# Kernel optimization log

Measured on AMD Instinct MI355X. Metric: run time of the kernel, lower is better.

The kernel has to match this reference:

```python
import jax, jax.numpy as jnp
import numpy as np

EPS = 1e-5  # nn.LayerNorm default

def _conv1x1(x, W):
    # x: (B,C,H,W), W: (O,C) -> (B,O,H,W)
    return jnp.einsum('bchw,oc->bohw', x, W)

def setup_inputs() -> dict:
    key = jax.random.key(0)
    kx, k1, k2, k3, k4, k5 = jax.random.split(key, 6)
    B, C, H, W = 16, 512, 64, 64
    inner = C // 2
    s = 1.0 / np.sqrt(C)
    return {
        'x':   jax.random.normal(kx, (B, C, H, W), dtype=jnp.float32),
        'Wsq': jax.random.normal(k1, (inner, C), dtype=jnp.float32) * s,
        'Wsv': jax.random.normal(k2, (inner, C), dtype=jnp.float32) * s,
        'Wcq': jax.random.normal(k3, (1, C), dtype=jnp.float32) * s,
        'Wcv': jax.random.normal(k4, (inner, C), dtype=jnp.float32) * s,
        'Wcz': jax.random.normal(k5, (C, inner), dtype=jnp.float32) * (1.0 / np.sqrt(inner)),
        'gamma': jnp.ones((C,), dtype=jnp.float32),
        'beta':  jnp.zeros((C,), dtype=jnp.float32),
    }

def _channel_pool(x, Wcq, Wcv, Wcz, gamma, beta):
    B, C, H, W = x.shape
    HW = H * W
    # channel_q: 1x1 conv to 1 channel -> (B, HW), softmax over HW
    cm = jnp.einsum('bchw,c->bhw', x, Wcq[0]).reshape(B, HW)
    cm = jax.nn.softmax(cm, axis=-1)                      # (B, HW)
    # channel_v: (B, inner, HW)
    iv = _conv1x1(x, Wcv).reshape(B, Wcv.shape[0], HW)
    context = jnp.einsum('bkn,bn->bk', iv, cm)            # (B, inner)
    z = jnp.einsum('bk,ok->bo', context, Wcz)             # (B, out)
    mu = jnp.mean(z, axis=-1, keepdims=True)
    var = jnp.mean((z - mu) ** 2, axis=-1, keepdims=True)
    zn = (z - mu) * jax.lax.rsqrt(var + EPS) * gamma + beta
    mask = jax.nn.sigmoid(zn)[:, :, None, None]           # (B, out, 1, 1)
    return x * mask

def _spatial_pool(x, Wsq, Wsv):
    B, C, H, W = x.shape
    HW = H * W
    g = _conv1x1(x, Wsq)                                  # (B, inner, H, W)
    avg = jnp.mean(g, axis=(2, 3))                        # (B, inner)
    avg = jax.nn.softmax(avg, axis=-1)                    # softmax over inner channels
    theta = _conv1x1(x, Wsv).reshape(B, Wsv.shape[0], HW) # (B, inner, HW)
    ctx = jnp.einsum('bk,bkn->bn', avg, theta).reshape(B, 1, H, W)
    return x * jax.nn.sigmoid(ctx)

def reference(x, Wsq, Wsv, Wcq, Wcv, Wcz, gamma, beta):
    # layout='parallel'
    ch = _channel_pool(x, Wcq, Wcv, Wcz, gamma, beta)
    sp = _spatial_pool(x, Wsq, Wsv)
    return ch + sp
```

## Files before the change

kernel.cpp:

```cpp
#include <hip/hip_runtime.h>
#include <math.h>

#define BB 16
#define CC 512
#define HWN 4096
#define INNER 256
#define EPSV 1e-5f

__device__ __forceinline__ float wave_sum(float s) {
    for (int off = 32; off; off >>= 1) s += __shfl_down(s, off);
    return s;
}
__device__ __forceinline__ float block_sum(float v, volatile float* s_red) {
    for (int off = 32; off; off >>= 1) v += __shfl_down(v, off);
    __syncthreads();
    if ((threadIdx.x & 63) == 0) s_red[threadIdx.x >> 6] = v;
    __syncthreads();
    return s_red[0] + s_red[1] + s_red[2] + s_red[3];
}
__device__ __forceinline__ float block_max(float v, volatile float* s_red) {
    for (int off = 32; off; off >>= 1) v = fmaxf(v, __shfl_down(v, off));
    __syncthreads();
    if ((threadIdx.x & 63) == 0) s_red[threadIdx.x >> 6] = v;
    __syncthreads();
    return fmaxf(fmaxf(s_red[0], s_red[1]), fmaxf(s_red[2], s_red[3]));
}
__device__ __forceinline__ float fsigmoid(float v) {
    return __builtin_amdgcn_rcpf(1.f + __expf(-v));
}

__global__ __launch_bounds__(256) void k1_pass(
    const float* __restrict__ x, const float* __restrict__ wcq,
    float* __restrict__ cm_logits, float* __restrict__ xsum)
{
    const int t = threadIdx.x, lane = t & 63, w = t >> 6;
    const int hw0 = blockIdx.x * 1024;
    const int c0  = blockIdx.y * 64;
    const int b   = blockIdx.z;
    __shared__ float s_w[64];
    __shared__ float s_red[4][1024];
    if (t < 64) s_w[t] = wcq[c0 + t];
    __syncthreads();

    const float* xb = x + ((size_t)b * CC + c0) * HWN + hw0 + lane * 4;
    float4 cm0 = {0,0,0,0}, cm1 = cm0, cm2 = cm0, cm3 = cm0;
    #pragma unroll 4
    for (int ci = 0; ci < 16; ++ci) {
        const int cl = w + ci * 4;
        const float* p = xb + (size_t)cl * HWN;
        float4 v0 = *(const float4*)(p);
        float4 v1 = *(const float4*)(p + 256);
        float4 v2 = *(const float4*)(p + 512);
        float4 v3 = *(const float4*)(p + 768);
        const float wc = s_w[cl];
        cm0.x = fmaf(v0.x, wc, cm0.x); cm0.y = fmaf(v0.y, wc, cm0.y);
        cm0.z = fmaf(v0.z, wc, cm0.z); cm0.w = fmaf(v0.w, wc, cm0.w);
        cm1.x = fmaf(v1.x, wc, cm1.x); cm1.y = fmaf(v1.y, wc, cm1.y);
        cm1.z = fmaf(v1.z, wc, cm1.z); cm1.w = fmaf(v1.w, wc, cm1.w);
        cm2.x = fmaf(v2.x, wc, cm2.x); cm2.y = fmaf(v2.y, wc, cm2.y);
        cm2.z = fmaf(v2.z, wc, cm2.z); cm2.w = fmaf(v2.w, wc, cm2.w);
        cm3.x = fmaf(v3.x, wc, cm3.x); cm3.y = fmaf(v3.y, wc, cm3.y);
        cm3.z = fmaf(v3.z, wc, cm3.z); cm3.w = fmaf(v3.w, wc, cm3.w);
        float s = (((v0.x+v0.y)+(v0.z+v0.w)) + ((v1.x+v1.y)+(v1.z+v1.w)))
                + (((v2.x+v2.y)+(v2.z+v2.w)) + ((v3.x+v3.y)+(v3.z+v3.w)));
        s = wave_sum(s);
        if (lane == 0) atomicAdd(&xsum[b * CC + c0 + cl], s);
    }
    *(float4*)&s_red[w][      lane*4] = cm0;
    *(float4*)&s_red[w][256 + lane*4] = cm1;
    *(float4*)&s_red[w][512 + lane*4] = cm2;
    *(float4*)&s_red[w][768 + lane*4] = cm3;
    __syncthreads();
    float4 r0 = *(float4*)&s_red[0][t*4];
    float4 r1 = *(float4*)&s_red[1][t*4];
    float4 r2 = *(float4*)&s_red[2][t*4];
    float4 r3 = *(float4*)&s_red[3][t*4];
    float* cp = cm_logits + b * HWN + hw0 + t * 4;
    atomicAdd(cp + 0, (r0.x + r1.x) + (r2.x + r3.x));
    atomicAdd(cp + 1, (r0.y + r1.y) + (r2.y + r3.y));
    atomicAdd(cp + 2, (r0.z + r1.z) + (r2.z + r3.z));
    atomicAdd(cp + 3, (r0.w + r1.w) + (r2.w + r3.w));
}

__global__ __launch_bounds__(256) void k2a_cmstats(
    const float* __restrict__ cm_logits, float* __restrict__ cmstats)
{
    const int b = blockIdx.x, t = threadIdx.x;
    __shared__ float s_red[4];
    const float* cl = cm_logits + b * HWN;
    float lmax = -1e30f;
    #pragma unroll 4
    for (int i = t; i < HWN; i += 256) lmax = fmaxf(lmax, cl[i]);
    lmax = block_max(lmax, s_red);
    float lsum = 0.f;
    #pragma unroll 4
    for (int i = t; i < HWN; i += 256) lsum += __expf(cl[i] - lmax);
    lsum = block_sum(lsum, s_red);
    if (t == 0) {
        cmstats[2 * b]     = lmax;
        cmstats[2 * b + 1] = __builtin_amdgcn_rcpf(lsum);
    }
}

__global__ __launch_bounds__(256) void k_mv512(
    const float* __restrict__ W, const float* __restrict__ v,
    float* __restrict__ y, float scale)
{
    const int b = blockIdx.x, t = threadIdx.x, lane = t & 63, w = t >> 6;
    const int k0 = blockIdx.y * 64;
    __shared__ float s_v[CC];
    s_v[t]       = v[b * CC + t];
    s_v[t + 256] = v[b * CC + t + 256];
    __syncthreads();
    float4 x0 = *(const float4*)&s_v[lane * 4];
    float4 x1 = *(const float4*)&s_v[256 + lane * 4];
    #pragma unroll 8
    for (int i = 0; i < 16; ++i) {
        const int k = k0 + w * 16 + i;
        const float* row = W + (size_t)k * CC + lane * 4;
        float4 q0 = *(const float4*)(row);
        float4 q1 = *(const float4*)(row + 256);
        float s = fmaf(q0.x,x0.x, fmaf(q0.y,x0.y, fmaf(q0.z,x0.z, q0.w*x0.w)))
                + fmaf(q1.x,x1.x, fmaf(q1.y,x1.y, fmaf(q1.z,x1.z, q1.w*x1.w)));
        s = wave_sum(s);
        if (lane == 0) y[b * INNER + k] = s * scale;
    }
}

__global__ __launch_bounds__(256) void k2c_wsv(
    const float* __restrict__ Wsv, const float* __restrict__ avg_logits,
    float* __restrict__ wsv_eff)
{
    const int b = blockIdx.x, t = threadIdx.x;
    const int c = blockIdx.y * 256 + t;
    __shared__ float s_red[4];
    __shared__ float s_avg[INNER];
    float a = avg_logits[b * INNER + t];
    float m = block_max(a, s_red);
    float e = __expf(a - m);
    float s2 = block_sum(e, s_red);
    s_avg[t] = e * __builtin_amdgcn_rcpf(s2);
    __syncthreads();
    float acc = 0.f;
    #pragma unroll 8
    for (int k = 0; k < INNER; ++k)
        acc = fmaf(s_avg[k], Wsv[(size_t)k * CC + c], acc);
    wsv_eff[b * CC + c] = acc;
}

__global__ __launch_bounds__(256) void k3_pass(
    const float* __restrict__ x, const float* __restrict__ wsv_eff,
    const float* __restrict__ cm_logits, const float* __restrict__ cmstats,
    float* __restrict__ ctx, float* __restrict__ xw)
{
    const int t = threadIdx.x, lane = t & 63, w = t >> 6;
    const int hw0 = blockIdx.x * 1024;
    const int c0  = blockIdx.y * 64;
    const int b   = blockIdx.z;
    __shared__ float s_w[64];
    __shared__ float s_red[4][1024];
    if (t < 64) s_w[t] = wsv_eff[b * CC + c0 + t];
    __syncthreads();

    const float cmax = cmstats[2 * b], crinv = cmstats[2 * b + 1];
    const float* mb = cm_logits + b * HWN + hw0 + lane * 4;
    float4 m0 = *(const float4*)(mb);
    float4 m1 = *(const float4*)(mb + 256);
    float4 m2 = *(const float4*)(mb + 512);
    float4 m3 = *(const float4*)(mb + 768);
    m0.x = __expf(m0.x - cmax) * crinv; m0.y = __expf(m0.y - cmax) * crinv;
    m0.z = __expf(m0.z - cmax) * crinv; m0.w = __expf(m0.w - cmax) * crinv;
    m1.x = __expf(m1.x - cmax) * crinv; m1.y = __expf(m1.y - cmax) * crinv;
    m1.z = __expf(m1.z - cmax) * crinv; m1.w = __expf(m1.w - cmax) * crinv;
    m2.x = __expf(m2.x - cmax) * crinv; m2.y = __expf(m2.y - cmax) * crinv;
    m2.z = __expf(m2.z - cmax) * crinv; m2.w = __expf(m2.w - cmax) * crinv;
    m3.x = __expf(m3.x - cmax) * crinv; m3.y = __expf(m3.y - cmax) * crinv;
    m3.z = __expf(m3.z - cmax) * crinv; m3.w = __expf(m3.w - cmax) * crinv;

    const float* xb = x + ((size_t)b * CC + c0) * HWN + hw0 + lane * 4;
    float4 a0 = {0,0,0,0}, a1 = a0, a2 = a0, a3 = a0;
    #pragma unroll 4
    for (int ci = 0; ci < 16; ++ci) {
        const int cl = w + ci * 4;
        const float* p = xb + (size_t)cl * HWN;
        float4 v0 = *(const float4*)(p);
        float4 v1 = *(const float4*)(p + 256);
        float4 v2 = *(const float4*)(p + 512);
        float4 v3 = *(const float4*)(p + 768);
        const float wc = s_w[cl];
        a0.x = fmaf(v0.x, wc, a0.x); a0.y = fmaf(v0.y, wc, a0.y);
        a0.z = fmaf(v0.z, wc, a0.z); a0.w = fmaf(v0.w, wc, a0.w);
        a1.x = fmaf(v1.x, wc, a1.x); a1.y = fmaf(v1.y, wc, a1.y);
        a1.z = fmaf(v1.z, wc, a1.z); a1.w = fmaf(v1.w, wc, a1.w);
        a2.x = fmaf(v2.x, wc, a2.x); a2.y = fmaf(v2.y, wc, a2.y);
        a2.z = fmaf(v2.z, wc, a2.z); a2.w = fmaf(v2.w, wc, a2.w);
        a3.x = fmaf(v3.x, wc, a3.x); a3.y = fmaf(v3.y, wc, a3.y);
        a3.z = fmaf(v3.z, wc, a3.z); a3.w = fmaf(v3.w, wc, a3.w);
        float s = fmaf(v0.x,m0.x, fmaf(v0.y,m0.y, fmaf(v0.z,m0.z, v0.w*m0.w)))
                + fmaf(v1.x,m1.x, fmaf(v1.y,m1.y, fmaf(v1.z,m1.z, v1.w*m1.w)))
                + fmaf(v2.x,m2.x, fmaf(v2.y,m2.y, fmaf(v2.z,m2.z, v2.w*m2.w)))
                + fmaf(v3.x,m3.x, fmaf(v3.y,m3.y, fmaf(v3.z,m3.z, v3.w*m3.w)));
        s = wave_sum(s);
        if (lane == 0) atomicAdd(&xw[b * CC + c0 + cl], s);
    }
    *(float4*)&s_red[w][      lane*4] = a0;
    *(float4*)&s_red[w][256 + lane*4] = a1;
    *(float4*)&s_red[w][512 + lane*4] = a2;
    *(float4*)&s_red[w][768 + lane*4] = a3;
    __syncthreads();
    float4 r0 = *(float4*)&s_red[0][t*4];
    float4 r1 = *(float4*)&s_red[1][t*4];
    float4 r2 = *(float4*)&s_red[2][t*4];
    float4 r3 = *(float4*)&s_red[3][t*4];
    float* cp = ctx + b * HWN + hw0 + t * 4;
    atomicAdd(cp + 0, (r0.x + r1.x) + (r2.x + r3.x));
    atomicAdd(cp + 1, (r0.y + r1.y) + (r2.y + r3.y));
    atomicAdd(cp + 2, (r0.z + r1.z) + (r2.z + r3.z));
    atomicAdd(cp + 3, (r0.w + r1.w) + (r2.w + r3.w));
}

__global__ __launch_bounds__(256) void k4b_z(
    const float* __restrict__ Wcz, const float* __restrict__ context,
    float* __restrict__ zbuf)
{
    const int b = blockIdx.x, t = threadIdx.x, lane = t & 63, w = t >> 6;
    const int o0 = blockIdx.y * 128;
    __shared__ float s_c[INNER];
    s_c[t] = context[b * INNER + t];
    __syncthreads();
    float4 cv = *(const float4*)&s_c[lane * 4];
    #pragma unroll 8
    for (int i = 0; i < 32; ++i) {
        const int o = o0 + w * 32 + i;
        float4 q = *(const float4*)(Wcz + (size_t)o * INNER + lane * 4);
        float s = fmaf(q.x,cv.x, fmaf(q.y,cv.y, fmaf(q.z,cv.z, q.w*cv.w)));
        s = wave_sum(s);
        if (lane == 0) zbuf[b * CC + o] = s;
    }
}

__global__ __launch_bounds__(256) void k4c_ln(
    const float* __restrict__ gamma, const float* __restrict__ beta,
    const float* __restrict__ zbuf, const float* __restrict__ ctx,
    float* __restrict__ mask, float* __restrict__ ctx_sig)
{
    const int b = blockIdx.x, t = threadIdx.x;
    __shared__ float s_red[4];
    float z0 = zbuf[b * CC + t], z1 = zbuf[b * CC + t + 256];
    float mu = block_sum(z0 + z1, s_red) * (1.f / CC);
    float d0 = z0 - mu, d1 = z1 - mu;
    float var = block_sum(d0 * d0 + d1 * d1, s_red) * (1.f / CC);
    float rstd = rsqrtf(var + EPSV);
    float zn0 = fmaf(d0 * rstd, gamma[t], beta[t]);
    float zn1 = fmaf(d1 * rstd, gamma[t + 256], beta[t + 256]);
    mask[b * CC + t]       = fsigmoid(zn0);
    mask[b * CC + t + 256] = fsigmoid(zn1);
    const float* ci = ctx + b * HWN;
    float* cs = ctx_sig + b * HWN;
    #pragma unroll 4
    for (int i = t; i < HWN; i += 256) cs[i] = fsigmoid(ci[i]);
}

__global__ __launch_bounds__(256) void k5_final(
    const float* __restrict__ x, const float* __restrict__ ctx_sig,
    const float* __restrict__ mask, float* __restrict__ out)
{
    const int t  = threadIdx.x;
    const int hw = blockIdx.x * 1024 + 4 * t;
    const int c  = blockIdx.y;
    const int b  = blockIdx.z;
    const float m = mask[b * CC + c];
    float4 s = *(const float4*)(ctx_sig + b * HWN + hw);
    const size_t base = ((size_t)b * CC + c) * HWN + hw;
    float4 xv = *(const float4*)(x + base);
    float4 o;
    o.x = xv.x * (m + s.x);
    o.y = xv.y * (m + s.y);
    o.z = xv.z * (m + s.z);
    o.w = xv.w * (m + s.w);
    *(float4*)(out + base) = o;
}

extern "C" void kernel_launch(void* const* d_in, const int* in_sizes, int n_in,
                              void* d_out, int out_size, void* d_ws, size_t ws_size,
                              hipStream_t stream) {
    const float* x     = (const float*)d_in[0];
    const float* Wsq   = (const float*)d_in[1];
    const float* Wsv   = (const float*)d_in[2];
    const float* Wcq   = (const float*)d_in[3];
    const float* Wcv   = (const float*)d_in[4];
    const float* Wcz   = (const float*)d_in[5];
    const float* gamma = (const float*)d_in[6];
    const float* beta  = (const float*)d_in[7];
    float* out = (float*)d_out;
    float* ws  = (float*)d_ws;

    float* cm_logits  = ws;
    float* ctx        = ws + 65536;
    float* xsum       = ws + 131072;
    float* xw         = ws + 139264;
    float* avg_logits = ws + 147456;
    float* wsv_eff    = ws + 151552;
    float* maskbuf    = ws + 159744;
    float* zbuf       = ws + 167936;
    float* context    = ws + 176128;
    float* ctx_sig    = ws + 180224;
    float* cmstats    = ws + 245760;

    hipMemsetAsync(d_ws, 0, 147456 * sizeof(float), stream);

    k1_pass<<<dim3(4, 8, BB), 256, 0, stream>>>(x, Wcq, cm_logits, xsum);
    k2a_cmstats<<<BB, 256, 0, stream>>>(cm_logits, cmstats);
    k_mv512<<<dim3(BB, 4), 256, 0, stream>>>(Wsq, xsum, avg_logits, 1.0f / HWN);
    k2c_wsv<<<dim3(BB, 2), 256, 0, stream>>>(Wsv, avg_logits, wsv_eff);
    k3_pass<<<dim3(4, 8, BB), 256, 0, stream>>>(x, wsv_eff, cm_logits, cmstats, ctx, xw);
    k_mv512<<<dim3(BB, 4), 256, 0, stream>>>(Wcv, xw, context, 1.0f);
    k4b_z<<<dim3(BB, 4), 256, 0, stream>>>(Wcz, context, zbuf);
    k4c_ln<<<BB, 256, 0, stream>>>(gamma, beta, zbuf, ctx, maskbuf, ctx_sig);
    k5_final<<<dim3(4, CC, BB), 256, 0, stream>>>(x, ctx_sig, maskbuf, out);
}
```

Measured before the change: 361.0 us.

## Replace atomics with partial buffers and fuse small stages into fewer kernels

The streaming passes over x now write per-block partial sums to disjoint buffers instead of using atomicAdd, which also removes the workspace memset. Blocks are retiled to 256 channels by 256 pixels. The softmax stats, the Wsq matvec, the channel softmax and the Wsv projection are fused into one per-batch kernel, and likewise the Wcv and Wcz matvecs and the LayerNorm. The final kernel now computes the spatial sigmoid inline and handles 16 channels per block. Launches and atomic contention go down, but the fused per-batch kernels run on only 16 blocks, so they have little parallelism.

```diff
diff --git a/kernel.cpp b/kernel.cpp
--- a/kernel.cpp
+++ b/kernel.cpp
@@ -29,256 +29,220 @@
     return __builtin_amdgcn_rcpf(1.f + __expf(-v));
 }
 
-__global__ __launch_bounds__(256) void k1_pass(
+__global__ __launch_bounds__(256) void kA(
     const float* __restrict__ x, const float* __restrict__ wcq,
-    float* __restrict__ cm_logits, float* __restrict__ xsum)
+    float* __restrict__ cm_part, float* __restrict__ xsum_part)
 {
     const int t = threadIdx.x, lane = t & 63, w = t >> 6;
-    const int hw0 = blockIdx.x * 1024;
-    const int c0  = blockIdx.y * 64;
+    const int hw0 = blockIdx.x * 256;
+    const int ch  = blockIdx.y;
+    const int c0  = ch * 256;
     const int b   = blockIdx.z;
-    __shared__ float s_w[64];
-    __shared__ float s_red[4][1024];
-    if (t < 64) s_w[t] = wcq[c0 + t];
-    __syncthreads();
-
+    __shared__ float s_w[256];
+    __shared__ float s_cm[4][256];
+    s_w[t] = wcq[c0 + t];
+    __syncthreads();
     const float* xb = x + ((size_t)b * CC + c0) * HWN + hw0 + lane * 4;
-    float4 cm0 = {0,0,0,0}, cm1 = cm0, cm2 = cm0, cm3 = cm0;
-    #pragma unroll 4
-    for (int ci = 0; ci < 16; ++ci) {
+    float* xsp = xsum_part + ((size_t)b * 16 + blockIdx.x) * CC + c0;
+    float4 acc = {0.f, 0.f, 0.f, 0.f};
+    #pragma unroll 8
+    for (int ci = 0; ci < 64; ++ci) {
         const int cl = w + ci * 4;
-        const float* p = xb + (size_t)cl * HWN;
-        float4 v0 = *(const float4*)(p);
-        float4 v1 = *(const float4*)(p + 256);
-        float4 v2 = *(const float4*)(p + 512);
-        float4 v3 = *(const float4*)(p + 768);
+        float4 v = *(const float4*)(xb + (size_t)cl * HWN);
         const float wc = s_w[cl];
-        cm0.x = fmaf(v0.x, wc, cm0.x); cm0.y = fmaf(v0.y, wc, cm0.y);
-        cm0.z = fmaf(v0.z, wc, cm0.z); cm0.w = fmaf(v0.w, wc, cm0.w);
-        cm1.x = fmaf(v1.x, wc, cm1.x); cm1.y = fmaf(v1.y, wc, cm1.y);
-        cm1.z = fmaf(v1.z, wc, cm1.z); cm1.w = fmaf(v1.w, wc, cm1.w);
-        cm2.x = fmaf(v2.x, wc, cm2.x); cm2.y = fmaf(v2.y, wc, cm2.y);
-        cm2.z = fmaf(v2.z, wc, cm2.z); cm2.w = fmaf(v2.w, wc, cm2.w);
-        cm3.x = fmaf(v3.x, wc, cm3.x); cm3.y = fmaf(v3.y, wc, cm3.y);
-        cm3.z = fmaf(v3.z, wc, cm3.z); cm3.w = fmaf(v3.w, wc, cm3.w);
-        float s = (((v0.x+v0.y)+(v0.z+v0.w)) + ((v1.x+v1.y)+(v1.z+v1.w)))
-                + (((v2.x+v2.y)+(v2.z+v2.w)) + ((v3.x+v3.y)+(v3.z+v3.w)));
-        s = wave_sum(s);
-        if (lane == 0) atomicAdd(&xsum[b * CC + c0 + cl], s);
-    }
-    *(float4*)&s_red[w][      lane*4] = cm0;
-    *(float4*)&s_red[w][256 + lane*4] = cm1;
-    *(float4*)&s_red[w][512 + lane*4] = cm2;
-    *(float4*)&s_red[w][768 + lane*4] = cm3;
-    __syncthreads();
-    float4 r0 = *(float4*)&s_red[0][t*4];
-    float4 r1 = *(float4*)&s_red[1][t*4];
-    float4 r2 = *(float4*)&s_red[2][t*4];
-    float4 r3 = *(float4*)&s_red[3][t*4];
-    float* cp = cm_logits + b * HWN + hw0 + t * 4;
-    atomicAdd(cp + 0, (r0.x + r1.x) + (r2.x + r3.x));
-    atomicAdd(cp + 1, (r0.y + r1.y) + (r2.y + r3.y));
-    atomicAdd(cp + 2, (r0.z + r1.z) + (r2.z + r3.z));
-    atomicAdd(cp + 3, (r0.w + r1.w) + (r2.w + r3.w));
-}
-
-__global__ __launch_bounds__(256) void k2a_cmstats(
-    const float* __restrict__ cm_logits, float* __restrict__ cmstats)
-{
-    const int b = blockIdx.x, t = threadIdx.x;
+        acc.x = fmaf(v.x, wc, acc.x); acc.y = fmaf(v.y, wc, acc.y);
+        acc.z = fmaf(v.z, wc, acc.z); acc.w = fmaf(v.w, wc, acc.w);
+        float s = (v.x + v.y) + (v.z + v.w);
+        s = wave_sum(s);
+        if (lane == 0) xsp[cl] = s;
+    }
+    *(float4*)&s_cm[w][lane * 4] = acc;
+    __syncthreads();
+    cm_part[((size_t)b * 2 + ch) * HWN + hw0 + t] =
+        (s_cm[0][t] + s_cm[1][t]) + (s_cm[2][t] + s_cm[3][t]);
+}
+
+__global__ __launch_bounds__(256) void kB(
+    const float* __restrict__ Wsq, const float* __restrict__ Wsv,
+    const float* __restrict__ cm_part, const float* __restrict__ xsum_part,
+    float* __restrict__ cmstats, float* __restrict__ wsv_eff)
+{
+    const int b = blockIdx.x, t = threadIdx.x, lane = t & 63, w = t >> 6;
     __shared__ float s_red[4];
-    const float* cl = cm_logits + b * HWN;
+    __shared__ float s_x[CC];
+    __shared__ float s_avg[INNER];
+    __shared__ float s_sm[INNER];
+    float a0 = 0.f, a1 = 0.f;
+    const float* xp = xsum_part + (size_t)b * 16 * CC;
+    #pragma unroll
+    for (int blk = 0; blk < 16; ++blk) {
+        a0 += xp[blk * CC + t];
+        a1 += xp[blk * CC + t + 256];
+    }
+    s_x[t] = a0; s_x[t + 256] = a1;
+    const float* c0p = cm_part + (size_t)b * 2 * HWN;
+    const float* c1p = c0p + HWN;
     float lmax = -1e30f;
     #pragma unroll 4
-    for (int i = t; i < HWN; i += 256) lmax = fmaxf(lmax, cl[i]);
+    for (int i = t; i < HWN; i += 256) lmax = fmaxf(lmax, c0p[i] + c1p[i]);
     lmax = block_max(lmax, s_red);
     float lsum = 0.f;
     #pragma unroll 4
-    for (int i = t; i < HWN; i += 256) lsum += __expf(cl[i] - lmax);
+    for (int i = t; i < HWN; i += 256) lsum += __expf(c0p[i] + c1p[i] - lmax);
     lsum = block_sum(lsum, s_red);
     if (t == 0) {
         cmstats[2 * b]     = lmax;
         cmstats[2 * b + 1] = __builtin_amdgcn_rcpf(lsum);
     }
-}
-
-__global__ __launch_bounds__(256) void k_mv512(
-    const float* __restrict__ W, const float* __restrict__ v,
-    float* __restrict__ y, float scale)
-{
-    const int b = blockIdx.x, t = threadIdx.x, lane = t & 63, w = t >> 6;
-    const int k0 = blockIdx.y * 64;
-    __shared__ float s_v[CC];
-    s_v[t]       = v[b * CC + t];
-    s_v[t + 256] = v[b * CC + t + 256];
-    __syncthreads();
-    float4 x0 = *(const float4*)&s_v[lane * 4];
-    float4 x1 = *(const float4*)&s_v[256 + lane * 4];
-    #pragma unroll 8
-    for (int i = 0; i < 16; ++i) {
-        const int k = k0 + w * 16 + i;
-        const float* row = W + (size_t)k * CC + lane * 4;
+    __syncthreads();
+    float4 x0 = *(const float4*)&s_x[lane * 4];
+    float4 x1 = *(const float4*)&s_x[256 + lane * 4];
+    for (int i = 0; i < 64; ++i) {
+        const int k = w * 64 + i;
+        const float* row = Wsq + (size_t)k * CC + lane * 4;
         float4 q0 = *(const float4*)(row);
         float4 q1 = *(const float4*)(row + 256);
         float s = fmaf(q0.x,x0.x, fmaf(q0.y,x0.y, fmaf(q0.z,x0.z, q0.w*x0.w)))
                 + fmaf(q1.x,x1.x, fmaf(q1.y,x1.y, fmaf(q1.z,x1.z, q1.w*x1.w)));
         s = wave_sum(s);
-        if (lane == 0) y[b * INNER + k] = s * scale;
-    }
-}
-
-__global__ __launch_bounds__(256) void k2c_wsv(
-    const float* __restrict__ Wsv, const float* __restrict__ avg_logits,
-    float* __restrict__ wsv_eff)
-{
-    const int b = blockIdx.x, t = threadIdx.x;
-    const int c = blockIdx.y * 256 + t;
-    __shared__ float s_red[4];
-    __shared__ float s_avg[INNER];
-    float a = avg_logits[b * INNER + t];
+        if (lane == 0) s_avg[k] = s * (1.0f / HWN);
+    }
+    __syncthreads();
+    float a = s_avg[t];
     float m = block_max(a, s_red);
     float e = __expf(a - m);
-    float s2 = block_sum(e, s_red);
-    s_avg[t] = e * __builtin_amdgcn_rcpf(s2);
-    __syncthreads();
-    float acc = 0.f;
+    float ssum = block_sum(e, s_red);
+    s_sm[t] = e * __builtin_amdgcn_rcpf(ssum);
+    __syncthreads();
+    float acc0 = 0.f, acc1 = 0.f;
     #pragma unroll 8
-    for (int k = 0; k < INNER; ++k)
-        acc = fmaf(s_avg[k], Wsv[(size_t)k * CC + c], acc);
-    wsv_eff[b * CC + c] = acc;
-}
-
-__global__ __launch_bounds__(256) void k3_pass(
+    for (int k = 0; k < INNER; ++k) {
+        const float sk = s_sm[k];
+        acc0 = fmaf(sk, Wsv[(size_t)k * CC + t],       acc0);
+        acc1 = fmaf(sk, Wsv[(size_t)k * CC + t + 256], acc1);
+    }
+    wsv_eff[b * CC + t]       = acc0;
+    wsv_eff[b * CC + t + 256] = acc1;
+}
+
+__global__ __launch_bounds__(256) void kC(
     const float* __restrict__ x, const float* __restrict__ wsv_eff,
-    const float* __restrict__ cm_logits, const float* __restrict__ cmstats,
-    float* __restrict__ ctx, float* __restrict__ xw)
+    const float* __restrict__ cm_part, const float* __restrict__ cmstats,
+    float* __restrict__ ctx_part, float* __restrict__ xw_part)
 {
     const int t = threadIdx.x, lane = t & 63, w = t >> 6;
-    const int hw0 = blockIdx.x * 1024;
-    const int c0  = blockIdx.y * 64;
+    const int hw0 = blockIdx.x * 256;
+    const int ch  = blockIdx.y;
+    const int c0  = ch * 256;
     const int b   = blockIdx.z;
-    __shared__ float s_w[64];
-    __shared__ float s_red[4][1024];
-    if (t < 64) s_w[t] = wsv_eff[b * CC + c0 + t];
-    __syncthreads();
-
+    __shared__ float s_w[256];
+    __shared__ float s_m[256];
+    __shared__ float s_cm[4][256];
+    s_w[t] = wsv_eff[b * CC + c0 + t];
     const float cmax = cmstats[2 * b], crinv = cmstats[2 * b + 1];
-    const float* mb = cm_logits + b * HWN + hw0 + lane * 4;
-    float4 m0 = *(const float4*)(mb);
-    float4 m1 = *(const float4*)(mb + 256);
-    float4 m2 = *(const float4*)(mb + 512);
-    float4 m3 = *(const float4*)(mb + 768);
-    m0.x = __expf(m0.x - cmax) * crinv; m0.y = __expf(m0.y - cmax) * crinv;
-    m0.z = __expf(m0.z - cmax) * crinv; m0.w = __expf(m0.w - cmax) * crinv;
-    m1.x = __expf(m1.x - cmax) * crinv; m1.y = __expf(m1.y - cmax) * crinv;
-    m1.z = __expf(m1.z - cmax) * crinv; m1.w = __expf(m1.w - cmax) * crinv;
-    m2.x = __expf(m2.x - cmax) * crinv; m2.y = __expf(m2.y - cmax) * crinv;
-    m2.z = __expf(m2.z - cmax) * crinv; m2.w = __expf(m2.w - cmax) * crinv;
-    m3.x = __expf(m3.x - cmax) * crinv; m3.y = __expf(m3.y - cmax) * crinv;
-    m3.z = __expf(m3.z - cmax) * crinv; m3.w = __expf(m3.w - cmax) * crinv;
-
+    const float cmv = cm_part[(size_t)b * 2 * HWN + hw0 + t]
+                    + cm_part[((size_t)b * 2 + 1) * HWN + hw0 + t];
+    s_m[t] = __expf(cmv - cmax) * crinv;
+    __syncthreads();
+    float4 mreg = *(const float4*)&s_m[lane * 4];
     const float* xb = x + ((size_t)b * CC + c0) * HWN + hw0 + lane * 4;
-    float4 a0 = {0,0,0,0}, a1 = a0, a2 = a0, a3 = a0;
-    #pragma unroll 4
-    for (int ci = 0; ci < 16; ++ci) {
+    float* xwp = xw_part + ((size_t)b * 16 + blockIdx.x) * CC + c0;
+    float4 acc = {0.f, 0.f, 0.f, 0.f};
+    #pragma unroll 8
+    for (int ci = 0; ci < 64; ++ci) {
         const int cl = w + ci * 4;
-        const float* p = xb + (size_t)cl * HWN;
-        float4 v0 = *(const float4*)(p);
-        float4 v1 = *(const float4*)(p + 256);
-        float4 v2 = *(const float4*)(p + 512);
-        float4 v3 = *(const float4*)(p + 768);
+        float4 v = *(const float4*)(xb + (size_t)cl * HWN);
         const float wc = s_w[cl];
-        a0.x = fmaf(v0.x, wc, a0.x); a0.y = fmaf(v0.y, wc, a0.y);
-        a0.z = fmaf(v0.z, wc, a0.z); a0.w = fmaf(v0.w, wc, a0.w);
-        a1.x = fmaf(v1.x, wc, a1.x); a1.y = fmaf(v1.y, wc, a1.y);
-        a1.z = fmaf(v1.z, wc, a1.z); a1.w = fmaf(v1.w, wc, a1.w);
-        a2.x = fmaf(v2.x, wc, a2.x); a2.y = fmaf(v2.y, wc, a2.y);
-        a2.z = fmaf(v2.z, wc, a2.z); a2.w = fmaf(v2.w, wc, a2.w);
-        a3.x = fmaf(v3.x, wc, a3.x); a3.y = fmaf(v3.y, wc, a3.y);
-        a3.z = fmaf(v3.z, wc, a3.z); a3.w = fmaf(v3.w, wc, a3.w);
-        float s = fmaf(v0.x,m0.x, fmaf(v0.y,m0.y, fmaf(v0.z,m0.z, v0.w*m0.w)))
-                + fmaf(v1.x,m1.x, fmaf(v1.y,m1.y, fmaf(v1.z,m1.z, v1.w*m1.w)))
-                + fmaf(v2.x,m2.x, fmaf(v2.y,m2.y, fmaf(v2.z,m2.z, v2.w*m2.w)))
-                + fmaf(v3.x,m3.x, fmaf(v3.y,m3.y, fmaf(v3.z,m3.z, v3.w*m3.w)));
-        s = wave_sum(s);
-        if (lane == 0) atomicAdd(&xw[b * CC + c0 + cl], s);
-    }
-    *(float4*)&s_red[w][      lane*4] = a0;
-    *(float4*)&s_red[w][256 + lane*4] = a1;
-    *(float4*)&s_red[w][512 + lane*4] = a2;
-    *(float4*)&s_red[w][768 + lane*4] = a3;
-    __syncthreads();
-    float4 r0 = *(float4*)&s_red[0][t*4];
-    float4 r1 = *(float4*)&s_red[1][t*4];
-    float4 r2 = *(float4*)&s_red[2][t*4];
-    float4 r3 = *(float4*)&s_red[3][t*4];
-    float* cp = ctx + b * HWN + hw0 + t * 4;
-    atomicAdd(cp + 0, (r0.x + r1.x) + (r2.x + r3.x));
-    atomicAdd(cp + 1, (r0.y + r1.y) + (r2.y + r3.y));
-    atomicAdd(cp + 2, (r0.z + r1.z) + (r2.z + r3.z));
-    atomicAdd(cp + 3, (r0.w + r1.w) + (r2.w + r3.w));
-}
-
-__global__ __launch_bounds__(256) void k4b_z(
-    const float* __restrict__ Wcz, const float* __restrict__ context,
-    float* __restrict__ zbuf)
+        acc.x = fmaf(v.x, wc, acc.x); acc.y = fmaf(v.y, wc, acc.y);
+        acc.z = fmaf(v.z, wc, acc.z); acc.w = fmaf(v.w, wc, acc.w);
+        float s = fmaf(v.x,mreg.x, fmaf(v.y,mreg.y, fmaf(v.z,mreg.z, v.w*mreg.w)));
+        s = wave_sum(s);
+        if (lane == 0) xwp[cl] = s;
+    }
+    *(float4*)&s_cm[w][lane * 4] = acc;
+    __syncthreads();
+    ctx_part[((size_t)b * 2 + ch) * HWN + hw0 + t] =
+        (s_cm[0][t] + s_cm[1][t]) + (s_cm[2][t] + s_cm[3][t]);
+}
+
+__global__ __launch_bounds__(256) void kD(
+    const float* __restrict__ Wcv, const float* __restrict__ Wcz,
+    const float* __restrict__ gamma, const float* __restrict__ beta,
+    const float* __restrict__ xw_part, float* __restrict__ maskbuf)
 {
     const int b = blockIdx.x, t = threadIdx.x, lane = t & 63, w = t >> 6;
-    const int o0 = blockIdx.y * 128;
-    __shared__ float s_c[INNER];
-    s_c[t] = context[b * INNER + t];
-    __syncthreads();
-    float4 cv = *(const float4*)&s_c[lane * 4];
-    #pragma unroll 8
-    for (int i = 0; i < 32; ++i) {
-        const int o = o0 + w * 32 + i;
+    __shared__ float s_red[4];
+    __shared__ float s_xw[CC];
+    __shared__ float s_ctx[INNER];
+    __shared__ float s_z[CC];
+    float a0 = 0.f, a1 = 0.f;
+    const float* xp = xw_part + (size_t)b * 16 * CC;
+    #pragma unroll
+    for (int blk = 0; blk < 16; ++blk) {
+        a0 += xp[blk * CC + t];
+        a1 += xp[blk * CC + t + 256];
+    }
+    s_xw[t] = a0; s_xw[t + 256] = a1;
+    __syncthreads();
+    float4 x0 = *(const float4*)&s_xw[lane * 4];
+    float4 x1 = *(const float4*)&s_xw[256 + lane * 4];
+    for (int i = 0; i < 64; ++i) {
+        const int k = w * 64 + i;
+        const float* row = Wcv + (size_t)k * CC + lane * 4;
+        float4 q0 = *(const float4*)(row);
+        float4 q1 = *(const float4*)(row + 256);
+        float s = fmaf(q0.x,x0.x, fmaf(q0.y,x0.y, fmaf(q0.z,x0.z, q0.w*x0.w)))
+                + fmaf(q1.x,x1.x, fmaf(q1.y,x1.y, fmaf(q1.z,x1.z, q1.w*x1.w)));
+        s = wave_sum(s);
+        if (lane == 0) s_ctx[k] = s;
+    }
+    __syncthreads();
+    float4 cv = *(const float4*)&s_ctx[lane * 4];
+    for (int i = 0; i < 128; ++i) {
+        const int o = w * 128 + i;
         float4 q = *(const float4*)(Wcz + (size_t)o * INNER + lane * 4);
         float s = fmaf(q.x,cv.x, fmaf(q.y,cv.y, fmaf(q.z,cv.z, q.w*cv.w)));
         s = wave_sum(s);
-        if (lane == 0) zbuf[b * CC + o] = s;
-    }
-}
-
-__global__ __launch_bounds__(256) void k4c_ln(
-    const float* __restrict__ gamma, const float* __restrict__ beta,
-    const float* __restrict__ zbuf, const float* __restrict__ ctx,
-    float* __restrict__ mask, float* __restrict__ ctx_sig)
-{
-    const int b = blockIdx.x, t = threadIdx.x;
-    __shared__ float s_red[4];
-    float z0 = zbuf[b * CC + t], z1 = zbuf[b * CC + t + 256];
+        if (lane == 0) s_z[o] = s;
+    }
+    __syncthreads();
+    float z0 = s_z[t], z1 = s_z[t + 256];
     float mu = block_sum(z0 + z1, s_red) * (1.f / CC);
     float d0 = z0 - mu, d1 = z1 - mu;
     float var = block_sum(d0 * d0 + d1 * d1, s_red) * (1.f / CC);
     float rstd = rsqrtf(var + EPSV);
-    float zn0 = fmaf(d0 * rstd, gamma[t], beta[t]);
-    float zn1 = fmaf(d1 * rstd, gamma[t + 256], beta[t + 256]);
-    mask[b * CC + t]       = fsigmoid(zn0);
-    mask[b * CC + t + 256] = fsigmoid(zn1);
-    const float* ci = ctx + b * HWN;
-    float* cs = ctx_sig + b * HWN;
+    maskbuf[b * CC + t]       = fsigmoid(fmaf(d0 * rstd, gamma[t],       beta[t]));
+    maskbuf[b * CC + t + 256] = fsigmoid(fmaf(d1 * rstd, gamma[t + 256], beta[t + 256]));
+}
+
+__global__ __launch_bounds__(256) void kE(
+    const float* __restrict__ x, const float* __restrict__ ctx_part,
+    const float* __restrict__ maskbuf, float* __restrict__ out)
+{
+    const int t  = threadIdx.x;
+    const int hw = blockIdx.x * 1024 + t * 4;
+    const int c0 = blockIdx.y * 16;
+    const int b  = blockIdx.z;
+    float4 p0 = *(const float4*)(ctx_part + ((size_t)b * 2)     * HWN + hw);
+    float4 p1 = *(const float4*)(ctx_part + ((size_t)b * 2 + 1) * HWN + hw);
+    float4 sg;
+    sg.x = fsigmoid(p0.x + p1.x);
+    sg.y = fsigmoid(p0.y + p1.y);
+    sg.z = fsigmoid(p0.z + p1.z);
+    sg.w = fsigmoid(p0.w + p1.w);
+    const float* mb = maskbuf + b * CC + c0;
+    const size_t base = ((size_t)b * CC + c0) * HWN + hw;
     #pragma unroll 4
-    for (int i = t; i < HWN; i += 256) cs[i] = fsigmoid(ci[i]);
-}
-
-__global__ __launch_bounds__(256) void k5_final(
-    const float* __restrict__ x, const float* __restrict__ ctx_sig,
-    const float* __restrict__ mask, float* __restrict__ out)
-{
-    const int t  = threadIdx.x;
-    const int hw = blockIdx.x * 1024 + 4 * t;
-    const int c  = blockIdx.y;
-    const int b  = blockIdx.z;
-    const float m = mask[b * CC + c];
-    float4 s = *(const float4*)(ctx_sig + b * HWN + hw);
-    const size_t base = ((size_t)b * CC + c) * HWN + hw;
-    float4 xv = *(const float4*)(x + base);
-    float4 o;
-    o.x = xv.x * (m + s.x);
-    o.y = xv.y * (m + s.y);
-    o.z = xv.z * (m + s.z);
-    o.w = xv.w * (m + s.w);
-    *(float4*)(out + base) = o;
+    for (int ci = 0; ci < 16; ++ci) {
+        const float m = mb[ci];
+        float4 xv = *(const float4*)(x + base + (size_t)ci * HWN);
+        float4 o;
+        o.x = xv.x * (m + sg.x);
+        o.y = xv.y * (m + sg.y);
+        o.z = xv.z * (m + sg.z);
+        o.w = xv.w * (m + sg.w);
+        *(float4*)(out + base + (size_t)ci * HWN) = o;
+    }
 }
 
 extern "C" void kernel_launch(void* const* d_in, const int* in_sizes, int n_in,
@@ -295,27 +259,16 @@
     float* out = (float*)d_out;
     float* ws  = (float*)d_ws;
 
-    float* cm_logits  = ws;
-    float* ctx        = ws + 65536;
-    float* xsum       = ws + 131072;
-    float* xw         = ws + 139264;
-    float* avg_logits = ws + 147456;
-    float* wsv_eff    = ws + 151552;
-    float* maskbuf    = ws + 159744;
-    float* zbuf       = ws + 167936;
-    float* context    = ws + 176128;
-    float* ctx_sig    = ws + 180224;
-    float* cmstats    = ws + 245760;
-
-    hipMemsetAsync(d_ws, 0, 147456 * sizeof(float), stream);
-
-    k1_pass<<<dim3(4, 8, BB), 256, 0, stream>>>(x, Wcq, cm_logits, xsum);
-    k2a_cmstats<<<BB, 256, 0, stream>>>(cm_logits, cmstats);
-    k_mv512<<<dim3(BB, 4), 256, 0, stream>>>(Wsq, xsum, avg_logits, 1.0f / HWN);
-    k2c_wsv<<<dim3(BB, 2), 256, 0, stream>>>(Wsv, avg_logits, wsv_eff);
-    k3_pass<<<dim3(4, 8, BB), 256, 0, stream>>>(x, wsv_eff, cm_logits, cmstats, ctx, xw);
-    k_mv512<<<dim3(BB, 4), 256, 0, stream>>>(Wcv, xw, context, 1.0f);
-    k4b_z<<<dim3(BB, 4), 256, 0, stream>>>(Wcz, context, zbuf);
-    k4c_ln<<<BB, 256, 0, stream>>>(gamma, beta, zbuf, ctx, maskbuf, ctx_sig);
-    k5_final<<<dim3(4, CC, BB), 256, 0, stream>>>(x, ctx_sig, maskbuf, out);
-}
+    float* cm_part   = ws;
+    float* xsum_part = ws + 131072;
+    float* ctx_part  = ws + 262144;
+    float* cmstats   = ws + 393216;
+    float* wsv_eff   = ws + 393248;
+    float* maskbuf   = ws + 401440;
+
+    kA<<<dim3(16, 2, BB), 256, 0, stream>>>(x, Wcq, cm_part, xsum_part);
+    kB<<<BB, 256, 0, stream>>>(Wsq, Wsv, cm_part, xsum_part, cmstats, wsv_eff);
+    kC<<<dim3(16, 2, BB), 256, 0, stream>>>(x, wsv_eff, cm_part, cmstats, ctx_part, xsum_part);
+    kD<<<BB, 256, 0, stream>>>(Wcv, Wcz, gamma, beta, xsum_part, maskbuf);
+    kE<<<dim3(4, 32, BB), 256, 0, stream>>>(x, ctx_part, maskbuf, out);
+}
```

New measurement: 503.0 us. +39.3%, slower.
